# Performance work log

Hardware: AMD Instinct MI355X
Metric: run time of the kernel (lower is better)

## Reference

```python
import jax, jax.numpy as jnp
import numpy as np

# Dims / scalars (from init_kwargs: m = int(T/dt), delta = dt, theta_star = threshold)
M = 50000
N = 500
DELTA = 0.001
GLEAK = 1.0
TAUS = 10.0
THETA_STAR = 1.0
SPIKE_PROB = 0.02  # sparse binary spike raster as produced by time2spike


def setup_inputs() -> dict:
    key = jax.random.key(0)
    k1, k2, k3 = jax.random.split(key, 3)
    # binary spike raster [m, n]
    spikes = (jax.random.uniform(k1, (M, N)) < SPIKE_PROB).astype(jnp.float32)
    # synapse weights ~ N(w_mean=0.01, 0.01)
    w = (0.01 + 0.01 * jax.random.normal(k2, (N,))).astype(jnp.float32)
    # reversal potentials: half excitatory (ex=5), half inhibitory (inh=-1), shuffled
    vrev = jnp.where(jax.random.uniform(k3, (N,)) < 0.5, 5.0, -1.0).astype(jnp.float32)
    return {"spikes": spikes, "w": w, "vrev": vrev}


def reference(spikes, w, vrev):
    dtype = spikes.dtype
    decay = jnp.exp(jnp.asarray(-1.0 / TAUS, dtype))

    # _compute_exp: exp_temp[i] = (exp_temp[i-1] + spikes[i-1]) * exp(-1/taus), exp_temp[0] = 0
    def exp_step(carry, s):
        nxt = (carry + s) * decay
        return nxt, nxt

    _, e_tail = jax.lax.scan(exp_step, jnp.zeros((N,), dtype), spikes[:-1])
    exp_temp = jnp.concatenate([jnp.zeros((1, N), dtype), e_tail], axis=0)  # [M, N]

    # Gsyn_pre = |w| * exp_temp ; Isyn_pre = Vrev * |w| * exp_temp.
    # Only their per-timestep sums over synapses enter the vtr recurrence,
    # so contract over n immediately instead of materializing [M, N] products.
    absw = jnp.abs(w)
    g_sum = exp_temp @ absw            # [M] = sum_j Gsyn_pre[i, j]
    i_sum = exp_temp @ (vrev * absw)   # [M] = sum_j Isyn_pre[i, j]
    a = DELTA * (GLEAK + g_sum)        # per-step leak+conductance factor
    b = DELTA * i_sum                  # per-step input drive

    # _computevtr: if vtr[i-1] < theta: vtr[i] = vtr[i-1]*(1 - a[i-1]) + b[i-1]
    # else vtr[i] stays 0 (state reset after threshold crossing), vtr[0] = 0.
    def vtr_step(v, ab):
        ai, bi = ab
        nxt = jnp.where(v < THETA_STAR, v * (1.0 - ai) + bi, jnp.asarray(0.0, dtype))
        return nxt, nxt

    _, v_tail = jax.lax.scan(vtr_step, jnp.asarray(0.0, dtype), (a[:-1], b[:-1]))
    vtr = jnp.concatenate([jnp.zeros((1,), dtype), v_tail])  # [M]
    return vtr
```

## Files before the change

kernel.cpp:

```cpp
#include <hip/hip_runtime.h>
#include <cmath>

namespace {
constexpr int NELEM  = 50000;
constexpr int NSYN   = 500;
constexpr int NQ4    = 125;
constexpr int T      = 1024;
constexpr int SBLK   = 49;
constexpr int SLOTS  = SBLK * T;
constexpr int CMAXC  = (NELEM - 1) >> 6;
constexpr int NCH_PAD = 784;
constexpr int MAXSEG = 4096;
constexpr int NGRP   = NELEM / 8;
constexpr double DELTA_D = 1.0e-3;
constexpr double THETA_D = 1.0;
constexpr float  DECAY_F = 0.90483741803595957311f;
}

struct WS {
    double2 rq[SLOTS];
    double  eAm[SLOTS], eAg[SLOTS], eAi[SLOTS];
    double  ePl[SLOTS], eQl[SLOTS];
    double  gAm[64], gAg[64], gAi[64];
    double  gPp[64], gPq[64];
    double  gmaxR[1024];
    double  gbndQ[MAXSEG];
    int     gbnd[MAXSEG];
    int     gnseg;
    int     pad;
    float   swv[SLOTS];
    float   iwv[SLOTS];
};

__global__ __launch_bounds__(256) void k_rowdot(
    const float* __restrict__ spikes,
    const float* __restrict__ w,
    const float* __restrict__ vrev,
    float* __restrict__ swv,
    float* __restrict__ iwv)
{
    const int lane = threadIdx.x & 63;
    const int wv   = threadIdx.x >> 6;
    const int rg   = blockIdx.x * 4 + wv;
    if (rg >= NGRP) return;
    const int row0 = rg * 8;

    const float4* __restrict__ w4 = reinterpret_cast<const float4*>(w);
    const float4* __restrict__ r4 = reinterpret_cast<const float4*>(vrev);
    const int j1 = lane;
    const int j2 = lane + 64;
    const bool has2 = (j2 < NQ4);
    float4 a1 = w4[j1], r1 = r4[j1];
    float4 aw1 = make_float4(fabsf(a1.x), fabsf(a1.y), fabsf(a1.z), fabsf(a1.w));
    float4 ar1 = make_float4(aw1.x * r1.x, aw1.y * r1.y, aw1.z * r1.z, aw1.w * r1.w);
    float4 aw2 = make_float4(0.f, 0.f, 0.f, 0.f), ar2 = aw2;
    if (has2) {
        float4 a2 = w4[j2], r2 = r4[j2];
        aw2 = make_float4(fabsf(a2.x), fabsf(a2.y), fabsf(a2.z), fabsf(a2.w));
        ar2 = make_float4(aw2.x * r2.x, aw2.y * r2.y, aw2.z * r2.z, aw2.w * r2.w);
    }

    float sp[8], ip[8];
#pragma unroll
    for (int r = 0; r < 8; ++r) {
        const float4* __restrict__ srow =
            reinterpret_cast<const float4*>(spikes + (size_t)(row0 + r) * NSYN);
        float4 s1 = srow[j1];
        float a = s1.x * aw1.x + s1.y * aw1.y + s1.z * aw1.z + s1.w * aw1.w;
        float b = s1.x * ar1.x + s1.y * ar1.y + s1.z * ar1.z + s1.w * ar1.w;
        if (has2) {
            float4 s2 = srow[j2];
            a += s2.x * aw2.x + s2.y * aw2.y + s2.z * aw2.z + s2.w * aw2.w;
            b += s2.x * ar2.x + s2.y * ar2.y + s2.z * ar2.z + s2.w * ar2.w;
        }
        sp[r] = a; ip[r] = b;
    }
#pragma unroll
    for (int d = 32; d > 0; d >>= 1) {
#pragma unroll
        for (int r = 0; r < 8; ++r) {
            sp[r] += __shfl_xor(sp[r], d);
            ip[r] += __shfl_xor(ip[r], d);
        }
    }
    if (lane == 0) {
        *reinterpret_cast<float4*>(swv + row0)     = make_float4(sp[0], sp[1], sp[2], sp[3]);
        *reinterpret_cast<float4*>(swv + row0 + 4) = make_float4(sp[4], sp[5], sp[6], sp[7]);
        *reinterpret_cast<float4*>(iwv + row0)     = make_float4(ip[0], ip[1], ip[2], ip[3]);
        *reinterpret_cast<float4*>(iwv + row0 + 4) = make_float4(ip[4], ip[5], ip[6], ip[7]);
    }
}

__global__ __launch_bounds__(1024) void k_scanA(const float* __restrict__ swv,
                                                const float* __restrict__ iwv,
                                                WS* __restrict__ ws)
{
    const int tid = threadIdx.x, lane = tid & 63, wv = tid >> 6, blk = blockIdx.x;
    const int idx = blk * T + tid;
    const bool live = (idx < NELEM);
    const double decay = (double)DECAY_F;
    __shared__ double s_a[16], s_b[16], s_c[16];

    double s = live ? (double)swv[idx] : 0.0;
    double t = live ? (double)iwv[idx] : 0.0;
    double m_in = live ? decay : 1.0;
    double g_in = live ? s * decay : 0.0;
    double i_in = live ? t * decay : 0.0;
#pragma unroll
    for (int d = 1; d < 64; d <<= 1) {
        double pm = __shfl_up(m_in, d);
        double pg = __shfl_up(g_in, d);
        double pi = __shfl_up(i_in, d);
        if (lane >= d) {
            g_in = m_in * pg + g_in;
            i_in = m_in * pi + i_in;
            m_in = pm * m_in;
        }
    }
    if (lane == 63) { s_a[wv] = m_in; s_b[wv] = g_in; s_c[wv] = i_in; }
    __syncthreads();
    if (wv == 0) {
        double wm = (lane < 16) ? s_a[lane] : 1.0;
        double wg = (lane < 16) ? s_b[lane] : 0.0;
        double wi = (lane < 16) ? s_c[lane] : 0.0;
#pragma unroll
        for (int d = 1; d < 16; d <<= 1) {
            double pm = __shfl_up(wm, d);
            double pg = __shfl_up(wg, d);
            double pi = __shfl_up(wi, d);
            if (lane >= d) {
                wg = wm * pg + wg;
                wi = wm * pi + wi;
                wm = pm * wm;
            }
        }
        if (lane < 16) { s_a[lane] = wm; s_b[lane] = wg; s_c[lane] = wi; }
        if (lane == 15) { ws->gAm[blk] = wm; ws->gAg[blk] = wg; ws->gAi[blk] = wi; }
    }
    __syncthreads();
    double em = __shfl_up(m_in, 1), eg = __shfl_up(g_in, 1), ei = __shfl_up(i_in, 1);
    if (lane == 0) { em = 1.0; eg = 0.0; ei = 0.0; }
    if (wv > 0) {
        double qm = s_a[wv - 1], qg = s_b[wv - 1], qi = s_c[wv - 1];
        eg = em * qg + eg;
        ei = em * qi + ei;
        em = qm * em;
    }
    ws->eAm[idx] = em; ws->eAg[idx] = eg; ws->eAi[idx] = ei;
}

__global__ __launch_bounds__(1024) void k_scanB(WS* __restrict__ ws)
{
    const int tid = threadIdx.x, lane = tid & 63, wv = tid >> 6, blk = blockIdx.x;
    const int idx = blk * T + tid;
    const bool live = (idx < NELEM);
    __shared__ double s_a[16], s_b[16];
    __shared__ double s_qg0, s_qi0;

    double em = ws->eAm[idx], eg = ws->eAg[idx], ei = ws->eAi[idx];

    if (wv == 0) {
        double am = (lane < SBLK) ? ws->gAm[lane] : 1.0;
        double ag = (lane < SBLK) ? ws->gAg[lane] : 0.0;
        double ai = (lane < SBLK) ? ws->gAi[lane] : 0.0;
#pragma unroll
        for (int d = 1; d < 64; d <<= 1) {
            double pm = __shfl_up(am, d);
            double pg = __shfl_up(ag, d);
            double pi = __shfl_up(ai, d);
            if (lane >= d) {
                ag = am * pg + ag;
                ai = am * pi + ai;
                am = pm * am;
            }
        }
        double zg = __shfl_up(ag, 1), zi = __shfl_up(ai, 1);
        if (lane == 0) { zg = 0.0; zi = 0.0; }
        if (lane == blk) { s_qg0 = zg; s_qi0 = zi; }
    }
    __syncthreads();

    double Eg = em * s_qg0 + eg;
    double Ei = em * s_qi0 + ei;
    double p_in = 1.0, q_in = 0.0;
    if (live) {
        double aa = DELTA_D * (1.0 + Eg);
        double om = 1.0 - aa;
        p_in = om;
        q_in = (DELTA_D * Ei) / om;
    }
#pragma unroll
    for (int d = 1; d < 64; d <<= 1) {
        double pp = __shfl_up(p_in, d);
        double pq = __shfl_up(q_in, d);
        if (lane >= d) {
            q_in = pq + q_in / pp;
            p_in = pp * p_in;
        }
    }
    if (lane == 63) { s_a[wv] = p_in; s_b[wv] = q_in; }
    __syncthreads();
    if (wv == 0) {
        double wp = (lane < 16) ? s_a[lane] : 1.0;
        double wq = (lane < 16) ? s_b[lane] : 0.0;
#pragma unroll
        for (int d = 1; d < 16; d <<= 1) {
            double pp = __shfl_up(wp, d);
            double pq = __shfl_up(wq, d);
            if (lane >= d) {
                wq = pq + wq / pp;
                wp = pp * wp;
            }
        }
        if (lane < 16) { s_a[lane] = wp; s_b[lane] = wq; }
        if (lane == 15) { ws->gPp[blk] = wp; ws->gPq[blk] = wq; }
    }
    __syncthreads();
    double ep = __shfl_up(p_in, 1), eq = __shfl_up(q_in, 1);
    if (lane == 0) { ep = 1.0; eq = 0.0; }
    if (wv > 0) {
        double ap = s_a[wv - 1], aq = s_b[wv - 1];
        eq = aq + eq / ap;
        ep = ap * ep;
    }
    ws->ePl[idx] = ep; ws->eQl[idx] = eq;
}

__global__ __launch_bounds__(1024) void k_apply(WS* __restrict__ ws)
{
    const int tid = threadIdx.x, lane = tid & 63, wv = tid >> 6, blk = blockIdx.x;
    const int idx = blk * T + tid;
    const bool live = (idx < NELEM);
    __shared__ double s_qp0, s_qq0;

    double pl = ws->ePl[idx], ql = ws->eQl[idx];

    if (wv == 0) {
        double ap = (lane < SBLK) ? ws->gPp[lane] : 1.0;
        double aq = (lane < SBLK) ? ws->gPq[lane] : 0.0;
#pragma unroll
        for (int d = 1; d < 64; d <<= 1) {
            double pp = __shfl_up(ap, d);
            double pq = __shfl_up(aq, d);
            if (lane >= d) {
                aq = pq + aq / pp;
                ap = pp * ap;
            }
        }
        double zp = __shfl_up(ap, 1), zq = __shfl_up(aq, 1);
        if (lane == 0) { zp = 1.0; zq = 0.0; }
        if (lane == blk) { s_qp0 = zp; s_qq0 = zq; }
    }
    __syncthreads();

    double Q = s_qq0 + ql / s_qp0;
    double P = s_qp0 * pl;
    double R = live ? (Q - THETA_D / P) : -1.0e308;
    ws->rq[idx] = make_double2(R, Q);
    double mR = R;
#pragma unroll
    for (int d = 32; d > 0; d >>= 1) mR = fmax(mR, __shfl_xor(mR, d));
    if (lane == 0) ws->gmaxR[idx >> 6] = mR;
}

__global__ __launch_bounds__(1024) void k_search(WS* __restrict__ ws)
{
    const int tid = threadIdx.x, blk = blockIdx.x;

    if (blk == 0) {
        __shared__ double smax[NCH_PAD];
        for (int c = tid; c < NCH_PAD; c += T)
            smax[c] = (c <= CMAXC) ? ws->gmaxR[c] : -1.0e308;
        __syncthreads();

        if (tid < 64) {
            const int lane = tid;
            int nseg = 1;
            if (lane == 0) { ws->gbnd[0] = 0; ws->gbndQ[0] = 0.0; }
            double Qr = 0.0;
            int pos = 1;
            while (pos < NELEM && nseg < MAXSEG) {
                int c = pos >> 6;
                int i0 = -1;
                double Qnb = 0.0;
                while (true) {
                    int cf = -1;
                    for (int cb = c; cb <= CMAXC; cb += 64) {
                        int cc = cb + lane;
                        bool qy = (cc <= CMAXC) && (smax[cc] >= Qr);
                        unsigned long long m = __ballot(qy);
                        if (m) { cf = cb + __builtin_ctzll(m); break; }
                    }
                    if (cf < 0) break;
                    int i = (cf << 6) + lane;
                    bool valid = (i >= pos) && (i < NELEM);
                    double2 rv = valid ? ws->rq[i] : make_double2(-1.0e308, 0.0);
                    unsigned long long m2 = __ballot(valid && (rv.x >= Qr));
                    if (m2) {
                        int r = __builtin_ctzll(m2);
                        i0 = (cf << 6) + r;
                        if (r < 63) Qnb = __shfl(rv.y, r + 1);
                        break;
                    }
                    c = cf + 1;
                    if (c > CMAXC) break;
                }
                if (i0 < 0) break;
                int nb = i0 + 1;
                if (nb >= NELEM) break;
                if ((i0 & 63) == 63) Qnb = ws->rq[nb].y;
                Qr = Qnb;
                if (lane == 0) { ws->gbnd[nseg] = nb; ws->gbndQ[nseg] = Qr; }
                nseg++;
                pos = nb + 1;
            }
            if (lane == 0) ws->gnseg = nseg;
        } else {
            double acc = 0.0;
            for (int i = tid; i < NELEM; i += 7 * T) acc += ws->rq[i].x;
            asm volatile("" :: "v"((float)acc));
        }
    } else if ((blk & 7) == 0) {
        const int p = blk >> 3;
        double acc = 0.0;
        for (int i = p * T + tid; i < NELEM; i += 7 * T) acc += ws->rq[i].x;
        asm volatile("" :: "v"((float)acc));
    }
}

__global__ __launch_bounds__(1024) void k_fill(const WS* __restrict__ ws,
                                               float* __restrict__ out)
{
    __shared__ int    sb[MAXSEG];
    __shared__ double sq[MAXSEG];
    __shared__ int    s_nseg;
    const int tid = threadIdx.x;
    if (tid == 0) s_nseg = ws->gnseg;
    __syncthreads();
    const int nseg = s_nseg;
    for (int i = tid; i < nseg; i += T) { sb[i] = ws->gbnd[i]; sq[i] = ws->gbndQ[i]; }
    __syncthreads();

    const int idx = blockIdx.x * T + tid;
    if (idx < NELEM) {
        int lo = 0, hi = nseg - 1;
        while (lo < hi) {
            int mid = (lo + hi + 1) >> 1;
            if (sb[mid] <= idx) lo = mid; else hi = mid - 1;
        }
        if (idx == sb[lo]) {
            out[idx] = 0.0f;
        } else {
            double2 v = ws->rq[idx];
            double P = THETA_D / (v.y - v.x);
            out[idx] = (float)(P * (v.y - sq[lo]));
        }
    }
}

extern "C" void kernel_launch(void* const* d_in, const int* in_sizes, int n_in,
                              void* d_out, int out_size, void* d_ws, size_t ws_size,
                              hipStream_t stream) {
    const float* spikes = (const float*)d_in[0];
    const float* w      = (const float*)d_in[1];
    const float* vrev   = (const float*)d_in[2];
    float* out = (float*)d_out;
    WS* ws = (WS*)d_ws;

    hipLaunchKernelGGL(k_rowdot, dim3((NGRP + 3) / 4), dim3(256), 0, stream,
                       spikes, w, vrev, ws->swv, ws->iwv);
    hipLaunchKernelGGL(k_scanA,  dim3(SBLK), dim3(T), 0, stream, ws->swv, ws->iwv, ws);
    hipLaunchKernelGGL(k_scanB,  dim3(SBLK), dim3(T), 0, stream, ws);
    hipLaunchKernelGGL(k_apply,  dim3(SBLK), dim3(T), 0, stream, ws);
    hipLaunchKernelGGL(k_search, dim3(56),   dim3(T), 0, stream, ws);
    hipLaunchKernelGGL(k_fill,   dim3(SBLK), dim3(T), 0, stream, ws, out);
}
```

Before: 197.0 us.

## Fuse three scan kernels into one with inter-block flag synchronization

```diff
diff --git a/kernel.cpp b/kernel.cpp
--- a/kernel.cpp
+++ b/kernel.cpp
@@ -19,26 +19,41 @@
 
 struct WS {
     double2 rq[SLOTS];
-    double  eAm[SLOTS], eAg[SLOTS], eAi[SLOTS];
-    double  ePl[SLOTS], eQl[SLOTS];
     double  gAm[64], gAg[64], gAi[64];
     double  gPp[64], gPq[64];
     double  gmaxR[1024];
     double  gbndQ[MAXSEG];
     int     gbnd[MAXSEG];
     int     gnseg;
-    int     pad;
+    int     flagA[64];
+    int     flagB[64];
     float   swv[SLOTS];
     float   iwv[SLOTS];
 };
+
+__device__ inline void pub_d(double* p, double v) {
+    __hip_atomic_store(reinterpret_cast<unsigned long long*>(p),
+                       __double_as_longlong(v),
+                       __ATOMIC_RELAXED, __HIP_MEMORY_SCOPE_AGENT);
+}
+__device__ inline double rd_d(const double* p) {
+    unsigned long long u =
+        __hip_atomic_load(reinterpret_cast<const unsigned long long*>(p),
+                          __ATOMIC_RELAXED, __HIP_MEMORY_SCOPE_AGENT);
+    return __longlong_as_double(u);
+}
 
 __global__ __launch_bounds__(256) void k_rowdot(
     const float* __restrict__ spikes,
     const float* __restrict__ w,
     const float* __restrict__ vrev,
-    float* __restrict__ swv,
-    float* __restrict__ iwv)
+    WS* __restrict__ ws)
 {
+    if (blockIdx.x == 0 && threadIdx.x < 128) {
+        const int l = threadIdx.x;
+        if (l < 64) ws->flagA[l] = 0; else ws->flagB[l - 64] = 0;
+    }
+
     const int lane = threadIdx.x & 63;
     const int wv   = threadIdx.x >> 6;
     const int rg   = blockIdx.x * 4 + wv;
@@ -84,25 +99,24 @@
         }
     }
     if (lane == 0) {
-        *reinterpret_cast<float4*>(swv + row0)     = make_float4(sp[0], sp[1], sp[2], sp[3]);
-        *reinterpret_cast<float4*>(swv + row0 + 4) = make_float4(sp[4], sp[5], sp[6], sp[7]);
-        *reinterpret_cast<float4*>(iwv + row0)     = make_float4(ip[0], ip[1], ip[2], ip[3]);
-        *reinterpret_cast<float4*>(iwv + row0 + 4) = make_float4(ip[4], ip[5], ip[6], ip[7]);
-    }
-}
-
-__global__ __launch_bounds__(1024) void k_scanA(const float* __restrict__ swv,
-                                                const float* __restrict__ iwv,
-                                                WS* __restrict__ ws)
+        *reinterpret_cast<float4*>(ws->swv + row0)     = make_float4(sp[0], sp[1], sp[2], sp[3]);
+        *reinterpret_cast<float4*>(ws->swv + row0 + 4) = make_float4(sp[4], sp[5], sp[6], sp[7]);
+        *reinterpret_cast<float4*>(ws->iwv + row0)     = make_float4(ip[0], ip[1], ip[2], ip[3]);
+        *reinterpret_cast<float4*>(ws->iwv + row0 + 4) = make_float4(ip[4], ip[5], ip[6], ip[7]);
+    }
+}
+
+__global__ __launch_bounds__(1024) void k_scan(WS* __restrict__ ws)
 {
     const int tid = threadIdx.x, lane = tid & 63, wv = tid >> 6, blk = blockIdx.x;
     const int idx = blk * T + tid;
     const bool live = (idx < NELEM);
     const double decay = (double)DECAY_F;
     __shared__ double s_a[16], s_b[16], s_c[16];
-
-    double s = live ? (double)swv[idx] : 0.0;
-    double t = live ? (double)iwv[idx] : 0.0;
+    __shared__ double s_qg0, s_qi0, s_qp0, s_qq0;
+
+    double s = live ? (double)ws->swv[idx] : 0.0;
+    double t = live ? (double)ws->iwv[idx] : 0.0;
     double m_in = live ? decay : 1.0;
     double g_in = live ? s * decay : 0.0;
     double i_in = live ? t * decay : 0.0;
@@ -119,6 +133,7 @@
     }
     if (lane == 63) { s_a[wv] = m_in; s_b[wv] = g_in; s_c[wv] = i_in; }
     __syncthreads();
+
     if (wv == 0) {
         double wm = (lane < 16) ? s_a[lane] : 1.0;
         double wg = (lane < 16) ? s_b[lane] : 0.0;
@@ -135,34 +150,17 @@
             }
         }
         if (lane < 16) { s_a[lane] = wm; s_b[lane] = wg; s_c[lane] = wi; }
-        if (lane == 15) { ws->gAm[blk] = wm; ws->gAg[blk] = wg; ws->gAi[blk] = wi; }
-    }
-    __syncthreads();
-    double em = __shfl_up(m_in, 1), eg = __shfl_up(g_in, 1), ei = __shfl_up(i_in, 1);
-    if (lane == 0) { em = 1.0; eg = 0.0; ei = 0.0; }
-    if (wv > 0) {
-        double qm = s_a[wv - 1], qg = s_b[wv - 1], qi = s_c[wv - 1];
-        eg = em * qg + eg;
-        ei = em * qi + ei;
-        em = qm * em;
-    }
-    ws->eAm[idx] = em; ws->eAg[idx] = eg; ws->eAi[idx] = ei;
-}
-
-__global__ __launch_bounds__(1024) void k_scanB(WS* __restrict__ ws)
-{
-    const int tid = threadIdx.x, lane = tid & 63, wv = tid >> 6, blk = blockIdx.x;
-    const int idx = blk * T + tid;
-    const bool live = (idx < NELEM);
-    __shared__ double s_a[16], s_b[16];
-    __shared__ double s_qg0, s_qi0;
-
-    double em = ws->eAm[idx], eg = ws->eAg[idx], ei = ws->eAi[idx];
-
-    if (wv == 0) {
-        double am = (lane < SBLK) ? ws->gAm[lane] : 1.0;
-        double ag = (lane < SBLK) ? ws->gAg[lane] : 0.0;
-        double ai = (lane < SBLK) ? ws->gAi[lane] : 0.0;
+        if (lane == 15) {
+            pub_d(&ws->gAm[blk], wm); pub_d(&ws->gAg[blk], wg); pub_d(&ws->gAi[blk], wi);
+            __hip_atomic_store(&ws->flagA[blk], 1, __ATOMIC_RELEASE, __HIP_MEMORY_SCOPE_AGENT);
+        }
+        double am = 1.0, ag = 0.0, ai = 0.0;
+        if (lane < SBLK) {
+            while (__hip_atomic_load(&ws->flagA[lane], __ATOMIC_ACQUIRE,
+                                     __HIP_MEMORY_SCOPE_AGENT) == 0)
+                __builtin_amdgcn_s_sleep(1);
+            am = rd_d(&ws->gAm[lane]); ag = rd_d(&ws->gAg[lane]); ai = rd_d(&ws->gAi[lane]);
+        }
 #pragma unroll
         for (int d = 1; d < 64; d <<= 1) {
             double pm = __shfl_up(am, d);
@@ -180,6 +178,14 @@
     }
     __syncthreads();
 
+    double em = __shfl_up(m_in, 1), eg = __shfl_up(g_in, 1), ei = __shfl_up(i_in, 1);
+    if (lane == 0) { em = 1.0; eg = 0.0; ei = 0.0; }
+    if (wv > 0) {
+        double qm = s_a[wv - 1], qg = s_b[wv - 1], qi = s_c[wv - 1];
+        eg = em * qg + eg;
+        ei = em * qi + ei;
+        em = qm * em;
+    }
     double Eg = em * s_qg0 + eg;
     double Ei = em * s_qi0 + ei;
     double p_in = 1.0, q_in = 0.0;
@@ -189,6 +195,8 @@
         p_in = om;
         q_in = (DELTA_D * Ei) / om;
     }
+    __syncthreads();
+
 #pragma unroll
     for (int d = 1; d < 64; d <<= 1) {
         double pp = __shfl_up(p_in, d);
@@ -200,6 +208,7 @@
     }
     if (lane == 63) { s_a[wv] = p_in; s_b[wv] = q_in; }
     __syncthreads();
+
     if (wv == 0) {
         double wp = (lane < 16) ? s_a[lane] : 1.0;
         double wq = (lane < 16) ? s_b[lane] : 0.0;
@@ -213,31 +222,17 @@
             }
         }
         if (lane < 16) { s_a[lane] = wp; s_b[lane] = wq; }
-        if (lane == 15) { ws->gPp[blk] = wp; ws->gPq[blk] = wq; }
-    }
-    __syncthreads();
-    double ep = __shfl_up(p_in, 1), eq = __shfl_up(q_in, 1);
-    if (lane == 0) { ep = 1.0; eq = 0.0; }
-    if (wv > 0) {
-        double ap = s_a[wv - 1], aq = s_b[wv - 1];
-        eq = aq + eq / ap;
-        ep = ap * ep;
-    }
-    ws->ePl[idx] = ep; ws->eQl[idx] = eq;
-}
-
-__global__ __launch_bounds__(1024) void k_apply(WS* __restrict__ ws)
-{
-    const int tid = threadIdx.x, lane = tid & 63, wv = tid >> 6, blk = blockIdx.x;
-    const int idx = blk * T + tid;
-    const bool live = (idx < NELEM);
-    __shared__ double s_qp0, s_qq0;
-
-    double pl = ws->ePl[idx], ql = ws->eQl[idx];
-
-    if (wv == 0) {
-        double ap = (lane < SBLK) ? ws->gPp[lane] : 1.0;
-        double aq = (lane < SBLK) ? ws->gPq[lane] : 0.0;
+        if (lane == 15) {
+            pub_d(&ws->gPp[blk], wp); pub_d(&ws->gPq[blk], wq);
+            __hip_atomic_store(&ws->flagB[blk], 1, __ATOMIC_RELEASE, __HIP_MEMORY_SCOPE_AGENT);
+        }
+        double ap = 1.0, aq = 0.0;
+        if (lane < SBLK) {
+            while (__hip_atomic_load(&ws->flagB[lane], __ATOMIC_ACQUIRE,
+                                     __HIP_MEMORY_SCOPE_AGENT) == 0)
+                __builtin_amdgcn_s_sleep(1);
+            ap = rd_d(&ws->gPp[lane]); aq = rd_d(&ws->gPq[lane]);
+        }
 #pragma unroll
         for (int d = 1; d < 64; d <<= 1) {
             double pp = __shfl_up(ap, d);
@@ -253,8 +248,15 @@
     }
     __syncthreads();
 
-    double Q = s_qq0 + ql / s_qp0;
-    double P = s_qp0 * pl;
+    double ep = __shfl_up(p_in, 1), eq = __shfl_up(q_in, 1);
+    if (lane == 0) { ep = 1.0; eq = 0.0; }
+    if (wv > 0) {
+        double ap2 = s_a[wv - 1], aq2 = s_b[wv - 1];
+        eq = aq2 + eq / ap2;
+        ep = ap2 * ep;
+    }
+    double Q = s_qq0 + eq / s_qp0;
+    double P = s_qp0 * ep;
     double R = live ? (Q - THETA_D / P) : -1.0e308;
     ws->rq[idx] = make_double2(R, Q);
     double mR = R;
@@ -368,10 +370,8 @@
     WS* ws = (WS*)d_ws;
 
     hipLaunchKernelGGL(k_rowdot, dim3((NGRP + 3) / 4), dim3(256), 0, stream,
-                       spikes, w, vrev, ws->swv, ws->iwv);
-    hipLaunchKernelGGL(k_scanA,  dim3(SBLK), dim3(T), 0, stream, ws->swv, ws->iwv, ws);
-    hipLaunchKernelGGL(k_scanB,  dim3(SBLK), dim3(T), 0, stream, ws);
-    hipLaunchKernelGGL(k_apply,  dim3(SBLK), dim3(T), 0, stream, ws);
+                       spikes, w, vrev, ws);
+    hipLaunchKernelGGL(k_scan,   dim3(SBLK), dim3(T), 0, stream, ws);
     hipLaunchKernelGGL(k_search, dim3(56),   dim3(T), 0, stream, ws);
     hipLaunchKernelGGL(k_fill,   dim3(SBLK), dim3(T), 0, stream, ws, out);
 }
```

After: 194.9 us. Within noise of the previous version (-1.1%).
